# Kernel tuning notes

Hardware: AMD Instinct MI355X
Metric: run time of the kernel (lower is better)

Reference implementation:

```python
import jax, jax.numpy as jnp
import numpy as np

NUM_HEADS = 8
WEIGHTS_DIM = 512
INPUT_DIM = 512
D_HEAD = WEIGHTS_DIM // NUM_HEADS


def setup_inputs() -> dict:
    key = jax.random.key(0)
    ks = jax.random.split(key, 9)
    B, S, D = 4, 2048, INPUT_DIM
    s_in = 1.0 / np.sqrt(D)
    s_w = 1.0 / np.sqrt(WEIGHTS_DIM)
    return {
        "x": jax.random.normal(ks[0], (B, S, D), dtype=jnp.float32),
        "Wq": jax.random.normal(ks[1], (D, WEIGHTS_DIM), dtype=jnp.float32) * s_in,
        "bq": jnp.zeros((WEIGHTS_DIM,), dtype=jnp.float32),
        "Wk": jax.random.normal(ks[2], (D, WEIGHTS_DIM), dtype=jnp.float32) * s_in,
        "bk": jnp.zeros((WEIGHTS_DIM,), dtype=jnp.float32),
        "Wv": jax.random.normal(ks[3], (D, WEIGHTS_DIM), dtype=jnp.float32) * s_in,
        "bv": jnp.zeros((WEIGHTS_DIM,), dtype=jnp.float32),
        "Wh": jax.random.normal(ks[4], (WEIGHTS_DIM, D), dtype=jnp.float32) * s_w,
        "bh": jnp.zeros((D,), dtype=jnp.float32),
    }


def _split_heads(t):
    # [B, S, Dm] -> [B, H, S, d_head]
    B, S, _ = t.shape
    return t.reshape(B, S, NUM_HEADS, D_HEAD).transpose(0, 2, 1, 3)


def reference(x, Wq, bq, Wk, bk, Wv, bv, Wh, bh):
    q = _split_heads(x @ Wq + bq)
    k = _split_heads(x @ Wk + bk)
    v = _split_heads(x @ Wv + bv)
    scale = 1.0 / jnp.sqrt(jnp.float32(D_HEAD))
    scores = jnp.einsum("bhqd,bhkd->bhqk", q, k) * scale  # [B,H,S,S]
    weights = jax.nn.softmax(scores, axis=-1)
    attn = jnp.einsum("bhqk,bhkd->bhqd", weights, v)
    B, H, S, d = attn.shape
    concat = attn.transpose(0, 2, 1, 3).reshape(B, S, H * d)
    return concat @ Wh + bh
```

## Files before the change

kernel.cpp:

```cpp
#include <hip/hip_runtime.h>
#include <stdint.h>

#define NB  4
#define SS  2048
#define DD  512
#define HH  8
#define DHH 64
#define MM  (NB * SS)

typedef __attribute__((ext_vector_type(8))) short bf16x8;
typedef __attribute__((ext_vector_type(4))) float f32x4;
typedef __attribute__((ext_vector_type(4))) short s16x4;

union fu32 { float f; unsigned u; };
union pfu  { uint4 u; bf16x8 v; };

static __device__ __forceinline__ short f2bf(float f) {
  fu32 a; a.f = f;
  unsigned u = a.u;
  return (short)((u + 0x7fffu + ((u >> 16) & 1u)) >> 16);
}
static __device__ __forceinline__ float bf2f(short s) {
  fu32 t; t.u = ((unsigned)(unsigned short)s) << 16;
  return t.f;
}

static __device__ __forceinline__ void async16(const void* g, void* l) {
  __builtin_amdgcn_global_load_lds(
      (__attribute__((address_space(1))) unsigned*)(void*)g,
      (__attribute__((address_space(3))) unsigned*)l, 16, 0, 0);
}

__global__ __launch_bounds__(256) void prep_kernel(
    const float* __restrict__ x, short* __restrict__ xb,
    const float* __restrict__ W0, const float* __restrict__ W1,
    const float* __restrict__ W2, const float* __restrict__ W3,
    short* __restrict__ T0, short* __restrict__ T1,
    short* __restrict__ T2, short* __restrict__ T3) {
  const int bid = blockIdx.x, tid = threadIdx.x;
  if (bid < 2048) {
    int i = (bid * 256 + tid) * 8;
    float4 v0 = *(const float4*)(x + i);
    float4 v1 = *(const float4*)(x + i + 4);
    bf16x8 o;
    o[0] = f2bf(v0.x); o[1] = f2bf(v0.y); o[2] = f2bf(v0.z); o[3] = f2bf(v0.w);
    o[4] = f2bf(v1.x); o[5] = f2bf(v1.y); o[6] = f2bf(v1.z); o[7] = f2bf(v1.w);
    *(bf16x8*)(xb + i) = o;
  } else {
    int z = bid - 2048;
    int widx = z >> 6, rem = z & 63;
    const float* W = widx == 0 ? W0 : widx == 1 ? W1 : widx == 2 ? W2 : W3;
    short*       T = widx == 0 ? T0 : widx == 1 ? T1 : widx == 2 ? T2 : T3;
    int n  = (rem & 7) * 64 + (tid & 63);
    int k0 = (rem >> 3) * 64 + (tid >> 6) * 16;
    bf16x8 t0, t1;
#pragma unroll
    for (int j = 0; j < 8; ++j) t0[j] = f2bf(W[(size_t)(k0 + j) * DD + n]);
#pragma unroll
    for (int j = 0; j < 8; ++j) t1[j] = f2bf(W[(size_t)(k0 + 8 + j) * DD + n]);
    *(bf16x8*)(T + (size_t)n * DD + k0)     = t0;
    *(bf16x8*)(T + (size_t)n * DD + k0 + 8) = t1;
  }
}

__global__ __launch_bounds__(256, 4) void gemm_qkv_kernel(
    const short* __restrict__ A, const short* __restrict__ Bt,
    const float* __restrict__ bq, const float* __restrict__ bk,
    const float* __restrict__ bv, short* __restrict__ qout,
    short* __restrict__ kout, short* __restrict__ vtout, float qscale) {
  __shared__ __align__(16) short a_sh[64 * 64];
  __shared__ __align__(16) short b_sh[128 * 64];
  const int tid  = threadIdx.x;
  const int w    = tid >> 6, lane = tid & 63, quad = lane >> 4, l16 = lane & 15;
  const int m0   = blockIdx.y * 64, n0 = blockIdx.x * 128;
  const int mw   = (w >> 1) * 32,   nw = (w & 1) * 64;
  const int rw   = lane >> 3, seg = lane & 7, gs = seg ^ rw;
  const int sxz  = l16 & 7;

  f32x4 acc[2][4];
#pragma unroll
  for (int i = 0; i < 2; ++i)
#pragma unroll
    for (int j = 0; j < 4; ++j) acc[i][j] = {0.f, 0.f, 0.f, 0.f};

  for (int kt = 0; kt < DD; kt += 64) {
    __syncthreads();
    {
      const short* ga = A  + (size_t)(m0 + w * 16 + rw) * DD + kt + gs * 8;
      const short* gb = Bt + (size_t)(n0 + w * 32 + rw) * DD + kt + gs * 8;
#pragma unroll
      for (int i = 0; i < 2; ++i)
        async16(ga + (size_t)i * 8 * DD, &a_sh[(w * 16 + i * 8) * 64]);
#pragma unroll
      for (int i = 0; i < 4; ++i)
        async16(gb + (size_t)i * 8 * DD, &b_sh[(w * 32 + i * 8) * 64]);
    }
    __syncthreads();
#pragma unroll
    for (int ks = 0; ks < 2; ++ks) {
      const int so = ((ks * 4 + quad) ^ sxz) * 8;
      bf16x8 af[2], bfr[4];
#pragma unroll
      for (int mt = 0; mt < 2; ++mt)
        af[mt] = *(const bf16x8*)&a_sh[(mw + mt * 16 + l16) * 64 + so];
#pragma unroll
      for (int nt = 0; nt < 4; ++nt)
        bfr[nt] = *(const bf16x8*)&b_sh[(nw + nt * 16 + l16) * 64 + so];
#pragma unroll
      for (int mt = 0; mt < 2; ++mt)
#pragma unroll
        for (int nt = 0; nt < 4; ++nt)
          acc[mt][nt] = __builtin_amdgcn_mfma_f32_16x16x32_bf16(
              af[mt], bfr[nt], acc[mt][nt], 0, 0, 0);
    }
  }

#pragma unroll
  for (int nt = 0; nt < 4; ++nt) {
    const int n   = n0 + nw + nt * 16 + l16;
    const int sg  = n >> 9, n9 = n & 511, h = n9 >> 6, d = n & 63;
    const float bval = (sg == 0 ? bq : sg == 1 ? bk : bv)[n9];
    const float scl  = (sg == 0) ? qscale : 1.0f;
#pragma unroll
    for (int mt = 0; mt < 2; ++mt) {
      const int mb = m0 + mw + mt * 16 + quad * 4;
      const int bi = mb >> 11, s = mb & (SS - 1);
      if (sg == 2) {
        s16x4 pk;
#pragma unroll
        for (int r = 0; r < 4; ++r) pk[r] = f2bf(acc[mt][nt][r] + bval);
        *(s16x4*)&vtout[((size_t)(bi * HH + h) * DHH + d) * SS + s] = pk;
      } else {
        short* o = (sg == 0) ? qout : kout;
        const size_t base = ((size_t)(bi * HH + h) * SS + s) * DHH + d;
#pragma unroll
        for (int r = 0; r < 4; ++r)
          o[base + (size_t)r * DHH] = f2bf((acc[mt][nt][r] + bval) * scl);
      }
    }
  }
}

__global__ __launch_bounds__(256, 4) void attn_kernel(
    const short* __restrict__ Qa, const short* __restrict__ Ka,
    const short* __restrict__ Vt, short* __restrict__ Op0,
    short* __restrict__ Op1, float* __restrict__ lpw) {
  __shared__ __align__(16) short k_sh[128 * 64];
  __shared__ __align__(16) short vt_sh[64 * 128];

  const int tid  = threadIdx.x;
  const int w    = tid >> 6, lane = tid & 63, quad = lane >> 4, l16 = lane & 15;
  const int n    = blockIdx.x;
  const int grp  = (n & 7) * 8 + (n >> 7);
  const int qt_b = (n >> 3) & 15;
  const int half = grp & 1, h = (grp >> 1) & 7, b = grp >> 4;
  const int q0   = qt_b * 128;
  const int rw = lane >> 3, seg = lane & 7, gs = seg ^ rw;
  const int sxz = l16 & 7;
  const size_t base = (size_t)(b * HH + h) * SS * DHH;
  const short* Qg = Qa + base + (size_t)(q0 + w * 32) * DHH;
  const short* Kg = Ka + base;
  const short* Vg = Vt + base;

  bf16x8 qf[2][2];
#pragma unroll
  for (int mt = 0; mt < 2; ++mt)
#pragma unroll
    for (int ks = 0; ks < 2; ++ks)
      qf[mt][ks] = *(const bf16x8*)(Qg + (size_t)(mt * 16 + l16) * DHH + ks * 32 + quad * 8);

  bf16x8 ones;
#pragma unroll
  for (int j = 0; j < 8; ++j) ones[j] = (short)0x3F80;

  f32x4 o_acc[2][4];
#pragma unroll
  for (int qt = 0; qt < 2; ++qt)
#pragma unroll
    for (int dt = 0; dt < 4; ++dt) o_acc[qt][dt] = {0.f, 0.f, 0.f, 0.f};
  f32x4 l_acc[2] = {{0.f, 0.f, 0.f, 0.f}, {0.f, 0.f, 0.f, 0.f}};

  const int addrA = ((((quad & 1) << 1) + (quad >> 1)) * 16 + l16) * 4;
  const int addrB = addrA ^ 64;
  const bool qeven = (quad & 1) == 0;

  const int kstart = half * (SS / 2);

  for (int kb = kstart; kb < kstart + SS / 2; kb += 128) {
    __syncthreads();
    {
      const short* gk = Kg + (size_t)(kb + w * 32 + rw) * DHH + gs * 8;
#pragma unroll
      for (int i = 0; i < 4; ++i)
        async16(gk + (size_t)i * 8 * DHH, &k_sh[(w * 32 + i * 8) * 64]);
#pragma unroll
      for (int i = 0; i < 4; ++i) {
        const int d = w * 16 + i * 4 + (lane >> 4);
        const int gseg = (lane & 15) ^ (d & 15);
        async16(Vg + (size_t)d * SS + kb + gseg * 8,
                &vt_sh[(w * 16 + i * 4) * 128]);
      }
    }
    __syncthreads();

#pragma unroll
    for (int ck = 0; ck < 4; ++ck) {
      uint2 pk[2][2];
#pragma unroll
      for (int t = 0; t < 2; ++t) {
        const int knt = ck * 2 + t;
        bf16x8 kf0 = *(const bf16x8*)&k_sh[(knt * 16 + l16) * 64 + ((0 * 4 + quad) ^ sxz) * 8];
        bf16x8 kf1 = *(const bf16x8*)&k_sh[(knt * 16 + l16) * 64 + ((1 * 4 + quad) ^ sxz) * 8];
#pragma unroll
        for (int qt = 0; qt < 2; ++qt) {
          f32x4 s = {0.f, 0.f, 0.f, 0.f};
          s = __builtin_amdgcn_mfma_f32_16x16x32_bf16(kf0, qf[qt][0], s, 0, 0, 0);
          s = __builtin_amdgcn_mfma_f32_16x16x32_bf16(kf1, qf[qt][1], s, 0, 0, 0);
          fu32 e0, e1, e2, e3;
          e0.f = __builtin_amdgcn_exp2f(s[0]);
          e1.f = __builtin_amdgcn_exp2f(s[1]);
          e2.f = __builtin_amdgcn_exp2f(s[2]);
          e3.f = __builtin_amdgcn_exp2f(s[3]);
          pk[qt][t].x = __builtin_amdgcn_perm(e1.u, e0.u, 0x07060302u);
          pk[qt][t].y = __builtin_amdgcn_perm(e3.u, e2.u, 0x07060302u);
        }
      }
      pfu pf[2];
#pragma unroll
      for (int qt = 0; qt < 2; ++qt) {
        unsigned p1x = (unsigned)__shfl_xor((int)pk[qt][1].x, 16);
        unsigned p1y = (unsigned)__shfl_xor((int)pk[qt][1].y, 16);
        unsigned v0x = qeven ? pk[qt][0].x : p1x;
        unsigned v0y = qeven ? pk[qt][0].y : p1y;
        unsigned v2x = qeven ? p1x : pk[qt][0].x;
        unsigned v2y = qeven ? p1y : pk[qt][0].y;
        pf[qt].u.x = (unsigned)__builtin_amdgcn_ds_bpermute(addrA, (int)v0x);
        pf[qt].u.y = (unsigned)__builtin_amdgcn_ds_bpermute(addrA, (int)v0y);
        pf[qt].u.z = (unsigned)__builtin_amdgcn_ds_bpermute(addrB, (int)v2x);
        pf[qt].u.w = (unsigned)__builtin_amdgcn_ds_bpermute(addrB, (int)v2y);
        l_acc[qt] = __builtin_amdgcn_mfma_f32_16x16x32_bf16(pf[qt].v, ones, l_acc[qt], 0, 0, 0);
      }
#pragma unroll
      for (int dt = 0; dt < 4; ++dt) {
        bf16x8 vf = *(const bf16x8*)&vt_sh[(dt * 16 + l16) * 128 + ((ck * 4 + quad) ^ l16) * 8];
        o_acc[0][dt] = __builtin_amdgcn_mfma_f32_16x16x32_bf16(pf[0].v, vf, o_acc[0][dt], 0, 0, 0);
        o_acc[1][dt] = __builtin_amdgcn_mfma_f32_16x16x32_bf16(pf[1].v, vf, o_acc[1][dt], 0, 0, 0);
      }
    }
  }

  short* Op = half ? Op1 : Op0;
#pragma unroll
  for (int qt = 0; qt < 2; ++qt) {
#pragma unroll
    for (int r = 0; r < 4; ++r) {
      const int qg = q0 + w * 32 + qt * 16 + quad * 4 + r;
      const size_t row = (size_t)(b * HH + h) * SS + qg;
      if (l16 == 0)
        lpw[(size_t)half * (NB * HH * SS) + row] = l_acc[qt][r];
      const float inv = __builtin_amdgcn_rcpf(l_acc[qt][r]);
#pragma unroll
      for (int dt = 0; dt < 4; ++dt)
        Op[row * DHH + dt * 16 + l16] = f2bf(o_acc[qt][dt][r] * inv);
    }
  }
}

__global__ void attn_combine_kernel(const short* __restrict__ Op0,
                                    const short* __restrict__ Op1,
                                    const float* __restrict__ lpw,
                                    short* __restrict__ aws) {
  int idx  = blockIdx.x * 256 + threadIdx.x;
  int dsg  = idx & 7;
  int row  = idx >> 3;
  int q    = row & (SS - 1);
  int bh   = row >> 11, h = bh & 7, b = bh >> 3;
  float l1 = lpw[row], l2 = lpw[NB * HH * SS + row];
  float inv = 1.f / (l1 + l2);
  float w1 = l1 * inv, w2 = l2 * inv;
  bf16x8 a = *(const bf16x8*)&Op0[(size_t)row * DHH + dsg * 8];
  bf16x8 c = *(const bf16x8*)&Op1[(size_t)row * DHH + dsg * 8];
  bf16x8 o;
#pragma unroll
  for (int j = 0; j < 8; ++j) o[j] = f2bf(w1 * bf2f(a[j]) + w2 * bf2f(c[j]));
  *(bf16x8*)&aws[((size_t)(b * SS + q)) * DD + h * DHH + dsg * 8] = o;
}

__global__ __launch_bounds__(256, 4) void gemm_proj_kernel(
    const short* __restrict__ A, const short* __restrict__ Bt,
    const float* __restrict__ bias, float* __restrict__ out) {
  __shared__ __align__(16) short a_sh[64 * 64];
  __shared__ __align__(16) short b_sh[64 * 64];
  const int tid = threadIdx.x;
  const int w   = tid >> 6, lane = tid & 63, quad = lane >> 4, l16 = lane & 15;
  const int m0  = blockIdx.y * 64, n0 = blockIdx.x * 64;
  const int mw  = (w >> 1) * 32, nw = (w & 1) * 32;
  const int rw  = lane >> 3, seg = lane & 7, gs = seg ^ rw;
  const int sxz = l16 & 7;

  f32x4 acc[2][2];
#pragma unroll
  for (int i = 0; i < 2; ++i)
#pragma unroll
    for (int j = 0; j < 2; ++j) acc[i][j] = {0.f, 0.f, 0.f, 0.f};

  for (int kt = 0; kt < DD; kt += 64) {
    __syncthreads();
    {
      const short* ga = A  + (size_t)(m0 + w * 16 + rw) * DD + kt + gs * 8;
      const short* gb = Bt + (size_t)(n0 + w * 16 + rw) * DD + kt + gs * 8;
#pragma unroll
      for (int i = 0; i < 2; ++i) {
        async16(ga + (size_t)i * 8 * DD, &a_sh[(w * 16 + i * 8) * 64]);
        async16(gb + (size_t)i * 8 * DD, &b_sh[(w * 16 + i * 8) * 64]);
      }
    }
    __syncthreads();
#pragma unroll
    for (int ks = 0; ks < 2; ++ks) {
      const int so = ((ks * 4 + quad) ^ sxz) * 8;
      bf16x8 af0 = *(const bf16x8*)&a_sh[(mw + l16) * 64 + so];
      bf16x8 af1 = *(const bf16x8*)&a_sh[(mw + 16 + l16) * 64 + so];
#pragma unroll
      for (int nt = 0; nt < 2; ++nt) {
        bf16x8 bfr = *(const bf16x8*)&b_sh[(nw + nt * 16 + l16) * 64 + so];
        acc[0][nt] = __builtin_amdgcn_mfma_f32_16x16x32_bf16(af0, bfr, acc[0][nt], 0, 0, 0);
        acc[1][nt] = __builtin_amdgcn_mfma_f32_16x16x32_bf16(af1, bfr, acc[1][nt], 0, 0, 0);
      }
    }
  }

#pragma unroll
  for (int nt = 0; nt < 2; ++nt) {
    const int   n  = n0 + nw + nt * 16 + l16;
    const float bv = bias[n];
#pragma unroll
    for (int mt = 0; mt < 2; ++mt)
#pragma unroll
      for (int r = 0; r < 4; ++r) {
        const int m = m0 + mw + mt * 16 + quad * 4 + r;
        out[(size_t)m * DD + n] = acc[mt][nt][r] + bv;
      }
  }
}

extern "C" void kernel_launch(void* const* d_in, const int* in_sizes, int n_in,
                              void* d_out, int out_size, void* d_ws, size_t ws_size,
                              hipStream_t stream) {
  (void)in_sizes; (void)n_in; (void)out_size; (void)ws_size;
  const float* x  = (const float*)d_in[0];
  const float* Wq = (const float*)d_in[1];
  const float* bq = (const float*)d_in[2];
  const float* Wk = (const float*)d_in[3];
  const float* bk = (const float*)d_in[4];
  const float* Wv = (const float*)d_in[5];
  const float* bv = (const float*)d_in[6];
  const float* Wh = (const float*)d_in[7];
  const float* bh = (const float*)d_in[8];

  short* ws  = (short*)d_ws;
  short* xb  = ws;
  short* wqt = xb  + (size_t)MM * DD;
  short* wkt = wqt + (size_t)DD * DD;
  short* wvt = wkt + (size_t)DD * DD;
  short* wht = wvt + (size_t)DD * DD;
  short* qws = wht + (size_t)DD * DD;
  short* kws = qws + (size_t)MM * DD;
  short* vws = kws + (size_t)MM * DD;
  short* aws = vws + (size_t)MM * DD;
  short* op1 = aws + (size_t)MM * DD;
  float* lpw = (float*)(op1 + (size_t)MM * DD);

  hipLaunchKernelGGL(prep_kernel, dim3(2048 + 256), dim3(256), 0, stream,
                     x, xb, Wq, Wk, Wv, Wh, wqt, wkt, wvt, wht);

  const float qscale = 1.4426950408889634f / 8.0f;
  hipLaunchKernelGGL(gemm_qkv_kernel, dim3(12, 128), dim3(256), 0, stream,
                     xb, wqt, bq, bk, bv, qws, kws, vws, qscale);

  hipLaunchKernelGGL(attn_kernel, dim3(1024), dim3(256), 0, stream,
                     qws, kws, vws, xb, op1, lpw);
  hipLaunchKernelGGL(attn_combine_kernel, dim3(NB * HH * SS * 8 / 256), dim3(256), 0, stream,
                     xb, op1, lpw, aws);

  hipLaunchKernelGGL(gemm_proj_kernel, dim3(8, 128), dim3(256), 0, stream,
                     aws, wht, bh, (float*)d_out);
}
```

Measured before the change: 171.2 us.

## Fuse split-KV attention combine into attention kernel via atomic ticket

Removes the separate combine kernel. Each attention block now increments a per-(batch, head, query-tile) atomic counter after writing its partial output. Whichever of the two halves finishes second reads the other half's partial output and normaliser, then writes the merged result straight into the concat buffer. This saves a kernel launch and a full pass over both partial outputs. In exchange it adds a memset, thread fences and an atomic per block, and the last block does scattered global reads.

Measured after the change: 384.8 us. 2.25x slower.

```diff
diff --git a/kernel.cpp b/kernel.cpp
--- a/kernel.cpp
+++ b/kernel.cpp
@@ -144,9 +144,11 @@
 __global__ __launch_bounds__(256, 4) void attn_kernel(
     const short* __restrict__ Qa, const short* __restrict__ Ka,
     const short* __restrict__ Vt, short* __restrict__ Op0,
-    short* __restrict__ Op1, float* __restrict__ lpw) {
+    short* __restrict__ Op1, float* __restrict__ lpw,
+    short* __restrict__ aws, unsigned* __restrict__ cnt) {
   __shared__ __align__(16) short k_sh[128 * 64];
   __shared__ __align__(16) short vt_sh[64 * 128];
+  __shared__ unsigned ticket_sh;
 
   const int tid  = threadIdx.x;
   const int w    = tid >> 6, lane = tid & 63, quad = lane >> 4, l16 = lane & 15;
@@ -264,26 +266,31 @@
         Op[row * DHH + dt * 16 + l16] = f2bf(o_acc[qt][dt][r] * inv);
     }
   }
-}
-
-__global__ void attn_combine_kernel(const short* __restrict__ Op0,
-                                    const short* __restrict__ Op1,
-                                    const float* __restrict__ lpw,
-                                    short* __restrict__ aws) {
-  int idx  = blockIdx.x * 256 + threadIdx.x;
-  int dsg  = idx & 7;
-  int row  = idx >> 3;
-  int q    = row & (SS - 1);
-  int bh   = row >> 11, h = bh & 7, b = bh >> 3;
-  float l1 = lpw[row], l2 = lpw[NB * HH * SS + row];
-  float inv = 1.f / (l1 + l2);
-  float w1 = l1 * inv, w2 = l2 * inv;
-  bf16x8 a = *(const bf16x8*)&Op0[(size_t)row * DHH + dsg * 8];
-  bf16x8 c = *(const bf16x8*)&Op1[(size_t)row * DHH + dsg * 8];
-  bf16x8 o;
-#pragma unroll
-  for (int j = 0; j < 8; ++j) o[j] = f2bf(w1 * bf2f(a[j]) + w2 * bf2f(c[j]));
-  *(bf16x8*)&aws[((size_t)(b * SS + q)) * DD + h * DHH + dsg * 8] = o;
+
+  __threadfence();
+  if (tid == 0) ticket_sh = atomicAdd(&cnt[(unsigned)((b * HH + h) * 16 + qt_b)], 1u);
+  __syncthreads();
+  if (ticket_sh == 1u) {
+    __threadfence();
+    const short* Pp = half ? Op0 : Op1;
+    const float* Pl = lpw + (size_t)(1 - half) * (NB * HH * SS);
+#pragma unroll
+    for (int qt = 0; qt < 2; ++qt) {
+#pragma unroll
+      for (int r = 0; r < 4; ++r) {
+        const int qg = q0 + w * 32 + qt * 16 + quad * 4 + r;
+        const size_t row = (size_t)(b * HH + h) * SS + qg;
+        const float l2  = Pl[row];
+        const float inv = __builtin_amdgcn_rcpf(l_acc[qt][r] + l2);
+#pragma unroll
+        for (int dt = 0; dt < 4; ++dt) {
+          const float pn = bf2f(Pp[row * DHH + dt * 16 + l16]);
+          const float c = (o_acc[qt][dt][r] + l2 * pn) * inv;
+          aws[(size_t)(b * SS + qg) * DD + h * DHH + dt * 16 + l16] = f2bf(c);
+        }
+      }
+    }
+  }
 }
 
 __global__ __launch_bounds__(256, 4) void gemm_proj_kernel(
@@ -370,6 +377,7 @@
   short* aws = vws + (size_t)MM * DD;
   short* op1 = aws + (size_t)MM * DD;
   float* lpw = (float*)(op1 + (size_t)MM * DD);
+  unsigned* cnt = (unsigned*)(lpw + 2 * (size_t)NB * HH * SS);
 
   hipLaunchKernelGGL(prep_kernel, dim3(2048 + 256), dim3(256), 0, stream,
                      x, xb, Wq, Wk, Wv, Wh, wqt, wkt, wvt, wht);
@@ -378,10 +386,10 @@
   hipLaunchKernelGGL(gemm_qkv_kernel, dim3(12, 128), dim3(256), 0, stream,
                      xb, wqt, bq, bk, bv, qws, kws, vws, qscale);
 
+  hipMemsetAsync(cnt, 0, 512 * sizeof(unsigned), stream);
+
   hipLaunchKernelGGL(attn_kernel, dim3(1024), dim3(256), 0, stream,
-                     qws, kws, vws, xb, op1, lpw);
-  hipLaunchKernelGGL(attn_combine_kernel, dim3(NB * HH * SS * 8 / 256), dim3(256), 0, stream,
-                     xb, op1, lpw, aws);
+                     qws, kws, vws, xb, op1, lpw, aws, cnt);
 
   hipLaunchKernelGGL(gemm_proj_kernel, dim3(8, 128), dim3(256), 0, stream,
                      aws, wht, bh, (float*)d_out);
```

## Fuse split-KV attention combine into output projection GEMM A-tile load

Applied to the files above, without the earlier changes.

Removes the separate attn_combine kernel. The projection GEMM now loads both partial attention outputs per head tile, computes the normalized combine weights from the stored row sums, and merges them into bf16 MFMA operands in registers. This drops one launch and the round-trip write and read of the combined attention buffer. The cost is that the proj kernel reads two A tiles, uses extra LDS, and recomputes the combine weights in every N-column block, so each combine is repeated 8 times.

New measurement: 172.8 us. About the same (+0.9%).

```diff
diff --git a/kernel.cpp b/kernel.cpp
--- a/kernel.cpp
+++ b/kernel.cpp
@@ -266,30 +266,12 @@
   }
 }
 
-__global__ void attn_combine_kernel(const short* __restrict__ Op0,
-                                    const short* __restrict__ Op1,
-                                    const float* __restrict__ lpw,
-                                    short* __restrict__ aws) {
-  int idx  = blockIdx.x * 256 + threadIdx.x;
-  int dsg  = idx & 7;
-  int row  = idx >> 3;
-  int q    = row & (SS - 1);
-  int bh   = row >> 11, h = bh & 7, b = bh >> 3;
-  float l1 = lpw[row], l2 = lpw[NB * HH * SS + row];
-  float inv = 1.f / (l1 + l2);
-  float w1 = l1 * inv, w2 = l2 * inv;
-  bf16x8 a = *(const bf16x8*)&Op0[(size_t)row * DHH + dsg * 8];
-  bf16x8 c = *(const bf16x8*)&Op1[(size_t)row * DHH + dsg * 8];
-  bf16x8 o;
-#pragma unroll
-  for (int j = 0; j < 8; ++j) o[j] = f2bf(w1 * bf2f(a[j]) + w2 * bf2f(c[j]));
-  *(bf16x8*)&aws[((size_t)(b * SS + q)) * DD + h * DHH + dsg * 8] = o;
-}
-
 __global__ __launch_bounds__(256, 4) void gemm_proj_kernel(
-    const short* __restrict__ A, const short* __restrict__ Bt,
+    const short* __restrict__ Op0, const short* __restrict__ Op1,
+    const float* __restrict__ lpw, const short* __restrict__ Bt,
     const float* __restrict__ bias, float* __restrict__ out) {
-  __shared__ __align__(16) short a_sh[64 * 64];
+  __shared__ __align__(16) short a0_sh[64 * 64];
+  __shared__ __align__(16) short a1_sh[64 * 64];
   __shared__ __align__(16) short b_sh[64 * 64];
   const int tid = threadIdx.x;
   const int w   = tid >> 6, lane = tid & 63, quad = lane >> 4, l16 = lane & 15;
@@ -297,6 +279,7 @@
   const int mw  = (w >> 1) * 32, nw = (w & 1) * 32;
   const int rw  = lane >> 3, seg = lane & 7, gs = seg ^ rw;
   const int sxz = l16 & 7;
+  const int bb  = m0 >> 11, q0 = m0 & (SS - 1);
 
   f32x4 acc[2][2];
 #pragma unroll
@@ -305,27 +288,53 @@
     for (int j = 0; j < 2; ++j) acc[i][j] = {0.f, 0.f, 0.f, 0.f};
 
   for (int kt = 0; kt < DD; kt += 64) {
+    const int h = kt >> 6;
+    const size_t lbase = (size_t)(bb * HH + h) * SS + q0;
+    const size_t abase = lbase * DHH;
     __syncthreads();
     {
-      const short* ga = A  + (size_t)(m0 + w * 16 + rw) * DD + kt + gs * 8;
+      const short* g0 = Op0 + abase + (size_t)(w * 16 + rw) * DHH + gs * 8;
+      const short* g1 = Op1 + abase + (size_t)(w * 16 + rw) * DHH + gs * 8;
       const short* gb = Bt + (size_t)(n0 + w * 16 + rw) * DD + kt + gs * 8;
 #pragma unroll
       for (int i = 0; i < 2; ++i) {
-        async16(ga + (size_t)i * 8 * DD, &a_sh[(w * 16 + i * 8) * 64]);
-        async16(gb + (size_t)i * 8 * DD, &b_sh[(w * 16 + i * 8) * 64]);
-      }
+        async16(g0 + (size_t)i * 8 * DHH, &a0_sh[(w * 16 + i * 8) * 64]);
+        async16(g1 + (size_t)i * 8 * DHH, &a1_sh[(w * 16 + i * 8) * 64]);
+        async16(gb + (size_t)i * 8 * DD,  &b_sh[(w * 16 + i * 8) * 64]);
+      }
+    }
+    float w1[2], w2[2];
+#pragma unroll
+    for (int mt = 0; mt < 2; ++mt) {
+      const size_t lrow = lbase + mw + mt * 16 + l16;
+      const float l1 = lpw[lrow];
+      const float l2 = lpw[(size_t)NB * HH * SS + lrow];
+      const float inv = __builtin_amdgcn_rcpf(l1 + l2);
+      w1[mt] = l1 * inv; w2[mt] = l2 * inv;
     }
     __syncthreads();
 #pragma unroll
     for (int ks = 0; ks < 2; ++ks) {
       const int so = ((ks * 4 + quad) ^ sxz) * 8;
-      bf16x8 af0 = *(const bf16x8*)&a_sh[(mw + l16) * 64 + so];
-      bf16x8 af1 = *(const bf16x8*)&a_sh[(mw + 16 + l16) * 64 + so];
+      pfu af[2];
+#pragma unroll
+      for (int mt = 0; mt < 2; ++mt) {
+        bf16x8 a0 = *(const bf16x8*)&a0_sh[(mw + mt * 16 + l16) * 64 + so];
+        bf16x8 a1 = *(const bf16x8*)&a1_sh[(mw + mt * 16 + l16) * 64 + so];
+        unsigned* rp = (unsigned*)&af[mt];
+#pragma unroll
+        for (int jp = 0; jp < 4; ++jp) {
+          fu32 f0, f1;
+          f0.f = w1[mt] * bf2f(a0[2 * jp])     + w2[mt] * bf2f(a1[2 * jp]);
+          f1.f = w1[mt] * bf2f(a0[2 * jp + 1]) + w2[mt] * bf2f(a1[2 * jp + 1]);
+          rp[jp] = __builtin_amdgcn_perm(f1.u, f0.u, 0x07060302u);
+        }
+      }
 #pragma unroll
       for (int nt = 0; nt < 2; ++nt) {
         bf16x8 bfr = *(const bf16x8*)&b_sh[(nw + nt * 16 + l16) * 64 + so];
-        acc[0][nt] = __builtin_amdgcn_mfma_f32_16x16x32_bf16(af0, bfr, acc[0][nt], 0, 0, 0);
-        acc[1][nt] = __builtin_amdgcn_mfma_f32_16x16x32_bf16(af1, bfr, acc[1][nt], 0, 0, 0);
+        acc[0][nt] = __builtin_amdgcn_mfma_f32_16x16x32_bf16(af[0].v, bfr, acc[0][nt], 0, 0, 0);
+        acc[1][nt] = __builtin_amdgcn_mfma_f32_16x16x32_bf16(af[1].v, bfr, acc[1][nt], 0, 0, 0);
       }
     }
   }
@@ -367,8 +376,7 @@
   short* qws = wht + (size_t)DD * DD;
   short* kws = qws + (size_t)MM * DD;
   short* vws = kws + (size_t)MM * DD;
-  short* aws = vws + (size_t)MM * DD;
-  short* op1 = aws + (size_t)MM * DD;
+  short* op1 = vws + (size_t)MM * DD;
   float* lpw = (float*)(op1 + (size_t)MM * DD);
 
   hipLaunchKernelGGL(prep_kernel, dim3(2048 + 256), dim3(256), 0, stream,
@@ -380,9 +388,7 @@
 
   hipLaunchKernelGGL(attn_kernel, dim3(1024), dim3(256), 0, stream,
                      qws, kws, vws, xb, op1, lpw);
-  hipLaunchKernelGGL(attn_combine_kernel, dim3(NB * HH * SS * 8 / 256), dim3(256), 0, stream,
-                     xb, op1, lpw, aws);
 
   hipLaunchKernelGGL(gemm_proj_kernel, dim3(8, 128), dim3(256), 0, stream,
-                     aws, wht, bh, (float*)d_out);
-}
+                     xb, op1, lpw, wht, bh, (float*)d_out);
+}
```
